# Optimization experiments

Hardware: AMD Instinct MI355X
Metric: run time of the kernel (lower is better)

Reference implementation:

```python
import jax, jax.numpy as jnp
import numpy as np

D_MODEL = 768
N_HEADS = 12
HEAD_DIM = D_MODEL // N_HEADS
NEG = -10000.0


def setup_inputs() -> dict:
    key = jax.random.key(0)
    ks = jax.random.split(key, 8)
    B, S, D = 2, 2048, D_MODEL
    inp = {
        "q": jax.random.normal(ks[0], (B, S, D), dtype=jnp.float32),
        "k": jax.random.normal(ks[1], (B, S, D), dtype=jnp.float32),
        "v": jax.random.normal(ks[2], (B, S, D), dtype=jnp.float32),
        "attn_mask": jax.random.randint(ks[3], (B, S), 0, 2, dtype=jnp.int32),
        # weights stored [in, out]; apply as x @ W (equivalent to torch Linear)
        "Wq": jax.random.normal(ks[4], (D, D), dtype=jnp.float32) / np.sqrt(D),
        "Wk": jax.random.normal(ks[5], (D, D), dtype=jnp.float32) / np.sqrt(D),
        "Wv": jax.random.normal(ks[6], (D, D), dtype=jnp.float32) / np.sqrt(D),
        "Wo": jax.random.normal(ks[7], (D, D), dtype=jnp.float32) / np.sqrt(D),
        "mask_future": 1,
    }
    return inp


def reference(q, k, v, attn_mask, Wq, Wk, Wv, Wo, mask_future):
    B, S, D = q.shape
    H, hd = N_HEADS, HEAD_DIM
    # project and split heads -> [B, H, S, hd]
    qh = (q @ Wq).reshape(B, S, H, hd).transpose(0, 2, 1, 3)
    kh = (k @ Wk).reshape(B, S, H, hd).transpose(0, 2, 1, 3)
    vh = (v @ Wv).reshape(B, S, H, hd).transpose(0, 2, 1, 3)

    scale = 1.0 / np.sqrt(hd).astype(np.float32)
    # full [B, H, L, S] score matrix (naive SDPA, as in the original)
    scores = jnp.einsum("bhld,bhsd->bhls", qh, kh) * scale
    if mask_future:
        causal = jnp.triu(jnp.full((S, S), NEG, dtype=scores.dtype), k=1)
        scores = scores + causal
    # padding mask: [B, S] -> broadcast over heads and query positions
    pad = attn_mask[:, None, None, :] == 0
    scores = jnp.where(pad, NEG, scores)
    attn = jax.nn.softmax(scores, axis=-1)  # dropout p=0.0 -> identity
    out = jnp.einsum("bhls,bhsd->bhld", attn, vh)  # [B, H, L, hd]
    out = out.transpose(0, 2, 1, 3).reshape(B, S, D)
    return out @ Wo
```

## Files before the change

### kernel.cpp

```cpp
#include <hip/hip_runtime.h>


#define NEGV (-10000.0f)

typedef __attribute__((ext_vector_type(8))) short v8s;
typedef __attribute__((ext_vector_type(4))) float v4f;
typedef __attribute__((ext_vector_type(8))) unsigned short v8u;

#define GLDS16(g, l)                                            \
  __builtin_amdgcn_global_load_lds(                             \
      (const __attribute__((address_space(1))) void*)(g),       \
      (__attribute__((address_space(3))) void*)(l), 16, 0, 0)

#define BAR()                                                   \
  do {                                                          \
    asm volatile("s_waitcnt lgkmcnt(0)" ::: "memory");          \
    __builtin_amdgcn_s_barrier();                               \
    __builtin_amdgcn_sched_barrier(0);                          \
  } while (0)

__device__ __forceinline__ unsigned short f2bf(float f) {
  unsigned int u = __float_as_uint(f);
  u += 0x7FFFu + ((u >> 16) & 1u);
  return (unsigned short)(u >> 16);
}

__device__ __forceinline__ unsigned int cvt_pk_bf16(float lo, float hi) {
  unsigned int r;
  asm("v_cvt_pk_bf16_f32 %0, %1, %2" : "=v"(r) : "v"(lo), "v"(hi));
  return r;
}

__global__ __launch_bounds__(256) void transpose_w(
    const float* __restrict__ w0, const float* __restrict__ w1,
    const float* __restrict__ w2, const float* __restrict__ w3,
    unsigned short* __restrict__ t0, unsigned short* __restrict__ t1,
    unsigned short* __restrict__ t2, unsigned short* __restrict__ t3) {
  const float* w; unsigned short* t;
  switch (blockIdx.z) {
    case 0: w = w0; t = t0; break;
    case 1: w = w1; t = t1; break;
    case 2: w = w2; t = t2; break;
    default: w = w3; t = t3; break;
  }
  __shared__ unsigned short tile[32][33];
  const int tx = threadIdx.x & 31, ty = threadIdx.x >> 5;
  const int x0 = blockIdx.x * 32, y0 = blockIdx.y * 32;
#pragma unroll
  for (int j = 0; j < 4; j++)
    tile[ty + j * 8][tx] = f2bf(w[(size_t)(y0 + ty + j * 8) * 768 + x0 + tx]);
  __syncthreads();
#pragma unroll
  for (int j = 0; j < 4; j++)
    t[(size_t)(x0 + ty + j * 8) * 768 + y0 + tx] = tile[tx][ty + j * 8];
}

__global__ __launch_bounds__(256) void transpose_vh(
    const unsigned short* __restrict__ vh, unsigned short* __restrict__ vht) {
  __shared__ unsigned short tile[32][33];
  const size_t hoff = (size_t)blockIdx.z * 2048 * 64;
  const unsigned short* src = vh + hoff;
  unsigned short* dst = vht + hoff;
  const int s0 = blockIdx.x * 32, d0 = blockIdx.y * 32;
  const int tx = threadIdx.x & 31, ty = threadIdx.x >> 5;
#pragma unroll
  for (int j = 0; j < 4; j++)
    tile[ty + j * 8][tx] = src[(size_t)(s0 + ty + j * 8) * 64 + d0 + tx];
  __syncthreads();
#pragma unroll
  for (int j = 0; j < 4; j++)
    dst[(size_t)(d0 + ty + j * 8) * 2048 + s0 + tx] = tile[tx][ty + j * 8];
}

template <bool ABF16HEAD, bool CF32ROW>
__device__ __forceinline__ void gemm_core(const void* __restrict__ A,
                                          const unsigned short* __restrict__ Wt,
                                          void* __restrict__ C) {
  const int tid = threadIdx.x;
  const int wave = tid >> 6, lane = tid & 63;
  const int quad = lane >> 4, l16 = lane & 15;
  const int wm = wave >> 1, wn = wave & 1;
  const int bm = blockIdx.x * 128, bn = blockIdx.y * 128;

  __shared__ __align__(16) unsigned short As[2][128 * 32];
  __shared__ __align__(16) unsigned short Bs[2][128 * 32];

  const int r0s = tid >> 2, c0s = (tid & 3) << 3;

  v4f acc[4][4];
#pragma unroll
  for (int i = 0; i < 4; i++)
#pragma unroll
    for (int j = 0; j < 4; j++) acc[i][j] = (v4f){0.f, 0.f, 0.f, 0.f};

  float4 nA00, nA01, nA10, nA11;

  auto issueB = [&](int kt, int nb) {
    const int c = kt * 32 + c0s;
    GLDS16(&Wt[(size_t)(bn + r0s) * 768 + c],
           &Bs[nb][(size_t)(wave * 64) * 8]);
    GLDS16(&Wt[(size_t)(bn + r0s + 64) * 768 + c],
           &Bs[nb][(size_t)(256 + wave * 64) * 8]);
  };
  auto issueA_glds = [&](int kt, int nb) {
    const int c = kt * 32 + c0s;
    const int rg0 = bm + r0s, rg1 = bm + r0s + 64;
    size_t a0 = ((size_t)((rg0 >> 11) * 12 + (c >> 6)) * 2048 +
                 (rg0 & 2047)) * 64 + (c & 63);
    size_t a1 = ((size_t)((rg1 >> 11) * 12 + (c >> 6)) * 2048 +
                 (rg1 & 2047)) * 64 + (c & 63);
    GLDS16((const unsigned short*)A + a0, &As[nb][(size_t)(wave * 64) * 8]);
    GLDS16((const unsigned short*)A + a1,
           &As[nb][(size_t)(256 + wave * 64) * 8]);
  };
  auto issueA_f32 = [&](int kt) {
    const float* Af = (const float*)A;
    const int c = kt * 32 + c0s;
    size_t a0 = (size_t)(bm + r0s) * 768 + c;
    size_t a1 = (size_t)(bm + r0s + 64) * 768 + c;
    nA00 = *(const float4*)(Af + a0);
    nA01 = *(const float4*)(Af + a0 + 4);
    nA10 = *(const float4*)(Af + a1);
    nA11 = *(const float4*)(Af + a1 + 4);
  };
  auto writeA_f32 = [&](int nb) {
    v8u t0, t1;
    t0[0] = f2bf(nA00.x); t0[1] = f2bf(nA00.y);
    t0[2] = f2bf(nA00.z); t0[3] = f2bf(nA00.w);
    t0[4] = f2bf(nA01.x); t0[5] = f2bf(nA01.y);
    t0[6] = f2bf(nA01.z); t0[7] = f2bf(nA01.w);
    t1[0] = f2bf(nA10.x); t1[1] = f2bf(nA10.y);
    t1[2] = f2bf(nA10.z); t1[3] = f2bf(nA10.w);
    t1[4] = f2bf(nA11.x); t1[5] = f2bf(nA11.y);
    t1[6] = f2bf(nA11.z); t1[7] = f2bf(nA11.w);
    *(uint4*)&As[nb][r0s * 32 + c0s] = *(uint4*)&t0;
    *(uint4*)&As[nb][(r0s + 64) * 32 + c0s] = *(uint4*)&t1;
  };

  if (ABF16HEAD) {
    issueA_glds(0, 0);
  } else {
    issueA_f32(0);
  }
  issueB(0, 0);
  if (!ABF16HEAD) writeA_f32(0);
  __syncthreads();

  for (int kt = 0; kt < 24; kt++) {
    const int cur = kt & 1, nxt = cur ^ 1;

    if (kt < 23) {
      if (ABF16HEAD) issueA_glds(kt + 1, nxt);
      else issueA_f32(kt + 1);
      issueB(kt + 1, nxt);
    }

    v8s aF[4], bF[4];
#pragma unroll
    for (int mt = 0; mt < 4; mt++)
      aF[mt] =
          *(const v8s*)&As[cur][(wm * 64 + mt * 16 + l16) * 32 + quad * 8];
#pragma unroll
    for (int nt = 0; nt < 4; nt++)
      bF[nt] =
          *(const v8s*)&Bs[cur][(wn * 64 + nt * 16 + l16) * 32 + quad * 8];
#pragma unroll
    for (int mt = 0; mt < 4; mt++)
#pragma unroll
      for (int nt = 0; nt < 4; nt++)
        acc[mt][nt] = __builtin_amdgcn_mfma_f32_16x16x32_bf16(
            aF[mt], bF[nt], acc[mt][nt], 0, 0, 0);

    if (kt < 23 && !ABF16HEAD) writeA_f32(nxt);
    __syncthreads();
  }

#pragma unroll
  for (int mt = 0; mt < 4; mt++) {
#pragma unroll
    for (int i = 0; i < 4; i++) {
      int row = bm + wm * 64 + mt * 16 + quad * 4 + i;
#pragma unroll
      for (int nt = 0; nt < 4; nt++) {
        int col = bn + wn * 64 + nt * 16 + l16;
        if (CF32ROW) {
          ((float*)C)[(size_t)row * 768 + col] = acc[mt][nt][i];
        } else {
          size_t off = ((size_t)((row >> 11) * 12 + (col >> 6)) * 2048 +
                        (row & 2047)) * 64 + (col & 63);
          ((unsigned short*)C)[off] = f2bf(acc[mt][nt][i]);
        }
      }
    }
  }
}

__global__ __launch_bounds__(256) void gemm_qkv(
    const float* __restrict__ xq, const float* __restrict__ xk,
    const float* __restrict__ xv, const unsigned short* __restrict__ wqt,
    const unsigned short* __restrict__ wkt, const unsigned short* __restrict__ wvt,
    unsigned short* __restrict__ qh, unsigned short* __restrict__ kh,
    unsigned short* __restrict__ vh) {
  const float* A; const unsigned short* Wt; unsigned short* C;
  switch (blockIdx.z) {
    case 0: A = xq; Wt = wqt; C = qh; break;
    case 1: A = xk; Wt = wkt; C = kh; break;
    default: A = xv; Wt = wvt; C = vh; break;
  }
  gemm_core<false, false>((const void*)A, Wt, (void*)C);
}

__global__ __launch_bounds__(256) void gemm_o(
    const unsigned short* __restrict__ oat, const unsigned short* __restrict__ wot,
    float* __restrict__ out) {
  gemm_core<true, true>((const void*)oat, wot, (void*)out);
}

__global__ __launch_bounds__(256) void attn_kernel(
    const unsigned short* __restrict__ qh, const unsigned short* __restrict__ kh,
    const unsigned short* __restrict__ vht, const int* __restrict__ attn_mask,
    const int* __restrict__ mask_future, unsigned short* __restrict__ o) {
  const int S = 2048, HD = 64, NH = 12;

  const int nlin = blockIdx.x + 32 * blockIdx.y;
  const int qt = (nlin >> 3) & 31;
  const int bh = (nlin & 7) * 3 + (nlin >> 8);
  const int b = bh / NH, h = bh % NH;

  const int tid = threadIdx.x;
  const int wave = tid >> 6, lane = tid & 63;
  const int quad = lane >> 4, l16 = lane & 15;

  __shared__ __align__(16) unsigned short Ks[2][64 * 72];
  __shared__ __align__(16) unsigned short Vt[2][64 * 72];
  __shared__ __align__(16) unsigned short Ps[4][16 * 72];
  __shared__ int s_flag;

  const size_t head_off = (size_t)(b * NH + h) * S * HD;
  const unsigned short* Kb = kh + head_off;
  const unsigned short* Vb = vht + head_off;

  const int mf = mask_future[0];
  if (tid == 0) s_flag = 0;

  const int qrow_l = qt * 64 + wave * 16 + l16;
  v8s aQ[2];
  {
    const unsigned short* qp = qh + head_off + (size_t)qrow_l * HD + quad * 8;
    aQ[0] = *(const v8s*)(qp);
    aQ[1] = *(const v8s*)(qp + 32);
  }
  const int qbase_D = qt * 64 + wave * 16 + quad * 4;

  float m_i = -1e30f;
  v4f accO[4], accL;
  accL = (v4f){0.f, 0.f, 0.f, 0.f};
#pragma unroll
  for (int dt = 0; dt < 4; dt++) accO[dt] = (v4f){0.f, 0.f, 0.f, 0.f};

  v8s ones;
#pragma unroll
  for (int j = 0; j < 8; j++) ones[j] = (short)0x3F80;

  const int kt_causal = mf ? qt : (S / 64 - 1);
  const int r0 = tid >> 3, c0s = (tid & 7) << 3;

  auto nexttile = [&](int t) -> int {
    if (t < kt_causal) return t + 1;
    if (t == kt_causal) return (mf && kt_causal < S / 64 - 1) ? t + 1 : -1;
    return (t < S / 64 - 1) ? t + 1 : -1;
  };

  uint4 pk0, pk1, pv0, pv1;
  int pmv = 0;
  unsigned long long msk0 = 0, msk1 = 0;
  int rtile = -1, stile = -1;

  auto prefetch = [&](int kt) {
    const uint4* srck = (const uint4*)(Kb + (size_t)kt * 64 * HD);
    pk0 = srck[tid];
    pk1 = srck[256 + tid];
    const unsigned short* vp = Vb + (size_t)r0 * S + kt * 64 + c0s;
    pv0 = *(const uint4*)vp;
    pv1 = *(const uint4*)(vp + (size_t)32 * S);
    pmv = attn_mask[b * S + kt * 64 + lane];
    rtile = kt;
  };

  auto stage = [&](int kb) {
    *(uint4*)&Ks[kb][r0 * 72 + c0s] = pk0;
    *(uint4*)&Ks[kb][(r0 + 32) * 72 + c0s] = pk1;
    *(uint4*)&Vt[kb][r0 * 72 + c0s] = pv0;
    *(uint4*)&Vt[kb][(r0 + 32) * 72 + c0s] = pv1;
    unsigned long long mk = __ballot(pmv != 0);
    if (kb) msk1 = mk; else msk0 = mk;
  };

  for (int phase = 0; phase < 2; phase++) {
    int kt_lo, kt_hi;
    if (phase == 0) { kt_lo = 0; kt_hi = kt_causal; }
    else {
      if (m_i < -5000.f) s_flag = 1;
      __syncthreads();
      if (!s_flag) break;
      kt_lo = kt_causal + 1; kt_hi = S / 64 - 1;
      if (kt_lo > kt_hi) break;
    }

    if (stile != kt_lo) {
      if (rtile != kt_lo) prefetch(kt_lo);
      stage(kt_lo & 1);
      stile = kt_lo;
      int nx = nexttile(kt_lo);
      if (nx >= 0) prefetch(nx);
    }

    for (int kt = kt_lo; kt <= kt_hi; kt++) {
      BAR();

      int nkt = nexttile(kt);
      if (nkt >= 0 && stile != nkt) {
        stage(nkt & 1);
        stile = nkt;
        int n2 = nexttile(nkt);
        if (n2 >= 0) prefetch(n2);
      }

      const int kb = kt & 1;
      const unsigned short* KsB = Ks[kb];
      const unsigned short* VtB = Vt[kb];
      const unsigned long long mk = kb ? msk1 : msk0;

      v4f sc[4];
      __builtin_amdgcn_s_setprio(1);
#pragma unroll
      for (int nt = 0; nt < 4; nt++) {
        const unsigned short* kp = &KsB[(nt * 16 + l16) * 72 + quad * 8];
        v8s k0 = *(const v8s*)kp;
        v8s k1 = *(const v8s*)(kp + 32);
        v4f z = (v4f){0.f, 0.f, 0.f, 0.f};
        z = __builtin_amdgcn_mfma_f32_16x16x32_bf16(k0, aQ[0], z, 0, 0, 0);
        z = __builtin_amdgcn_mfma_f32_16x16x32_bf16(k1, aQ[1], z, 0, 0, 0);
        sc[nt] = z;
      }
      __builtin_amdgcn_s_setprio(0);

#pragma unroll
      for (int nt = 0; nt < 4; nt++) {
#pragma unroll
        for (int i = 0; i < 4; i++) {
          int kid = nt * 16 + quad * 4 + i;
          int key = kt * 64 + kid;
          float v = sc[nt][i] * 0.125f;
          v += (mf && (key > qrow_l)) ? NEGV : 0.f;
          v = ((mk >> kid) & 1ull) ? v : NEGV;
          sc[nt][i] = v;
        }
      }

      float mx;
      {
        float a = fmaxf(fmaxf(sc[0][0], sc[0][1]), fmaxf(sc[0][2], sc[0][3]));
        float b2 = fmaxf(fmaxf(sc[1][0], sc[1][1]), fmaxf(sc[1][2], sc[1][3]));
        float c = fmaxf(fmaxf(sc[2][0], sc[2][1]), fmaxf(sc[2][2], sc[2][3]));
        float d = fmaxf(fmaxf(sc[3][0], sc[3][1]), fmaxf(sc[3][2], sc[3][3]));
        mx = fmaxf(fmaxf(a, b2), fmaxf(c, d));
      }
      mx = fmaxf(mx, __shfl_xor(mx, 16));
      mx = fmaxf(mx, __shfl_xor(mx, 32));

      if (!__all(mx - m_i <= 8.0f)) {
        float mnew = fmaxf(m_i, mx);
        float alpha = __expf(m_i - mnew);
        m_i = mnew;
        float a0 = __shfl(alpha, quad * 4 + 0);
        float a1 = __shfl(alpha, quad * 4 + 1);
        float a2 = __shfl(alpha, quad * 4 + 2);
        float a3 = __shfl(alpha, quad * 4 + 3);
#pragma unroll
        for (int dt = 0; dt < 4; dt++) {
          accO[dt][0] *= a0; accO[dt][1] *= a1;
          accO[dt][2] *= a2; accO[dt][3] *= a3;
        }
        accL[0] *= a0; accL[1] *= a1; accL[2] *= a2; accL[3] *= a3;
      }

#pragma unroll
      for (int nt = 0; nt < 4; nt++) {
#pragma unroll
        for (int i = 0; i < 4; i++)
          sc[nt][i] = __expf(sc[nt][i] - m_i);
        uint2 w;
        w.x = cvt_pk_bf16(sc[nt][0], sc[nt][1]);
        w.y = cvt_pk_bf16(sc[nt][2], sc[nt][3]);
        *(uint2*)&Ps[wave][l16 * 72 + nt * 16 + quad * 4] = w;
      }

      __builtin_amdgcn_s_setprio(1);
#pragma unroll
      for (int ks = 0; ks < 2; ks++) {
        v8s aP = *(const v8s*)&Ps[wave][l16 * 72 + ks * 32 + quad * 8];
        accL = __builtin_amdgcn_mfma_f32_16x16x32_bf16(aP, ones, accL, 0, 0, 0);
#pragma unroll
        for (int dt = 0; dt < 4; dt++) {
          v8s bV = *(const v8s*)&VtB[(dt * 16 + l16) * 72 + ks * 32 + quad * 8];
          accO[dt] =
              __builtin_amdgcn_mfma_f32_16x16x32_bf16(aP, bV, accO[dt], 0, 0, 0);
        }
      }
      __builtin_amdgcn_s_setprio(0);
    }
    if (phase == 0) __syncthreads();
  }

#pragma unroll
  for (int i = 0; i < 4; i++) {
    float inv = 1.f / accL[i];
    int qr = qbase_D + i;
    size_t base = head_off + (size_t)qr * HD;
#pragma unroll
    for (int dt = 0; dt < 4; dt++)
      o[base + dt * 16 + l16] = f2bf(accO[dt][i] * inv);
  }
}

extern "C" void kernel_launch(void* const* d_in, const int* in_sizes, int n_in,
                              void* d_out, int out_size, void* d_ws, size_t ws_size,
                              hipStream_t stream) {
  const float* q  = (const float*)d_in[0];
  const float* k  = (const float*)d_in[1];
  const float* v  = (const float*)d_in[2];
  const int* amask = (const int*)d_in[3];
  const float* Wq = (const float*)d_in[4];
  const float* Wk = (const float*)d_in[5];
  const float* Wv = (const float*)d_in[6];
  const float* Wo = (const float*)d_in[7];
  const int* mf  = (const int*)d_in[8];
  float* out = (float*)d_out;

  unsigned short* ws = (unsigned short*)d_ws;
  unsigned short* qh = ws;
  unsigned short* kh = qh + 3145728;
  unsigned short* vh = kh + 3145728;
  unsigned short* wqt = vh + 3145728;
  unsigned short* wkt = wqt + 589824;
  unsigned short* wvt = wkt + 589824;
  unsigned short* wot = wvt + 589824;
  unsigned short* vht = (unsigned short*)d_out;

  transpose_w<<<dim3(24, 24, 4), 256, 0, stream>>>(Wq, Wk, Wv, Wo,
                                                   wqt, wkt, wvt, wot);
  gemm_qkv<<<dim3(32, 6, 3), 256, 0, stream>>>(q, k, v, wqt, wkt, wvt,
                                               qh, kh, vh);
  transpose_vh<<<dim3(64, 2, 24), 256, 0, stream>>>(vh, vht);
  attn_kernel<<<dim3(32, 24), 256, 0, stream>>>(qh, kh, vht, amask, mf, qh);
  gemm_o<<<dim3(32, 6), 256, 0, stream>>>(qh, wot, out);
}
```

Baseline: 215.0 us.

## Schedule attention work items dynamically via atomic counter, longest-first

Replaces the static block-to-tile mapping in the attention kernel with a persistent-style loop that pulls work items from a global atomic counter. Items are ordered so that the longest causal query tiles run first, aiming to balance the triangular workload across CUs. The counter is reset inside the preceding transpose kernel. Each item costs an extra atomic plus a barrier, and blocks that exit early still occupy launch slots.

```diff
diff --git a/kernel.cpp b/kernel.cpp
--- a/kernel.cpp
+++ b/kernel.cpp
@@ -56,7 +56,11 @@
 }
 
 __global__ __launch_bounds__(256) void transpose_vh(
-    const unsigned short* __restrict__ vh, unsigned short* __restrict__ vht) {
+    const unsigned short* __restrict__ vh, unsigned short* __restrict__ vht,
+    int* __restrict__ ctr) {
+  if (blockIdx.x == 0 && blockIdx.y == 0 && blockIdx.z == 0 &&
+      threadIdx.x == 0)
+    *ctr = 0;
   __shared__ unsigned short tile[32][33];
   const size_t hoff = (size_t)blockIdx.z * 2048 * 64;
   const unsigned short* src = vh + hoff;
@@ -219,13 +223,9 @@
 __global__ __launch_bounds__(256) void attn_kernel(
     const unsigned short* __restrict__ qh, const unsigned short* __restrict__ kh,
     const unsigned short* __restrict__ vht, const int* __restrict__ attn_mask,
-    const int* __restrict__ mask_future, unsigned short* __restrict__ o) {
+    const int* __restrict__ mask_future, int* __restrict__ ctr,
+    unsigned short* __restrict__ o) {
   const int S = 2048, HD = 64, NH = 12;
-
-  const int nlin = blockIdx.x + 32 * blockIdx.y;
-  const int qt = (nlin >> 3) & 31;
-  const int bh = (nlin & 7) * 3 + (nlin >> 8);
-  const int b = bh / NH, h = bh % NH;
 
   const int tid = threadIdx.x;
   const int wave = tid >> 6, lane = tid & 63;
@@ -235,192 +235,208 @@
   __shared__ __align__(16) unsigned short Vt[2][64 * 72];
   __shared__ __align__(16) unsigned short Ps[4][16 * 72];
   __shared__ int s_flag;
-
-  const size_t head_off = (size_t)(b * NH + h) * S * HD;
-  const unsigned short* Kb = kh + head_off;
-  const unsigned short* Vb = vht + head_off;
+  __shared__ int s_item;
 
   const int mf = mask_future[0];
-  if (tid == 0) s_flag = 0;
-
-  const int qrow_l = qt * 64 + wave * 16 + l16;
-  v8s aQ[2];
-  {
-    const unsigned short* qp = qh + head_off + (size_t)qrow_l * HD + quad * 8;
-    aQ[0] = *(const v8s*)(qp);
-    aQ[1] = *(const v8s*)(qp + 32);
-  }
-  const int qbase_D = qt * 64 + wave * 16 + quad * 4;
-
-  float m_i = -1e30f;
-  v4f accO[4], accL;
-  accL = (v4f){0.f, 0.f, 0.f, 0.f};
-#pragma unroll
-  for (int dt = 0; dt < 4; dt++) accO[dt] = (v4f){0.f, 0.f, 0.f, 0.f};
+  const int r0 = tid >> 3, c0s = (tid & 7) << 3;
 
   v8s ones;
 #pragma unroll
   for (int j = 0; j < 8; j++) ones[j] = (short)0x3F80;
 
-  const int kt_causal = mf ? qt : (S / 64 - 1);
-  const int r0 = tid >> 3, c0s = (tid & 7) << 3;
-
-  auto nexttile = [&](int t) -> int {
-    if (t < kt_causal) return t + 1;
-    if (t == kt_causal) return (mf && kt_causal < S / 64 - 1) ? t + 1 : -1;
-    return (t < S / 64 - 1) ? t + 1 : -1;
-  };
-
-  uint4 pk0, pk1, pv0, pv1;
-  int pmv = 0;
-  unsigned long long msk0 = 0, msk1 = 0;
-  int rtile = -1, stile = -1;
-
-  auto prefetch = [&](int kt) {
-    const uint4* srck = (const uint4*)(Kb + (size_t)kt * 64 * HD);
-    pk0 = srck[tid];
-    pk1 = srck[256 + tid];
-    const unsigned short* vp = Vb + (size_t)r0 * S + kt * 64 + c0s;
-    pv0 = *(const uint4*)vp;
-    pv1 = *(const uint4*)(vp + (size_t)32 * S);
-    pmv = attn_mask[b * S + kt * 64 + lane];
-    rtile = kt;
-  };
-
-  auto stage = [&](int kb) {
-    *(uint4*)&Ks[kb][r0 * 72 + c0s] = pk0;
-    *(uint4*)&Ks[kb][(r0 + 32) * 72 + c0s] = pk1;
-    *(uint4*)&Vt[kb][r0 * 72 + c0s] = pv0;
-    *(uint4*)&Vt[kb][(r0 + 32) * 72 + c0s] = pv1;
-    unsigned long long mk = __ballot(pmv != 0);
-    if (kb) msk1 = mk; else msk0 = mk;
-  };
-
-  for (int phase = 0; phase < 2; phase++) {
-    int kt_lo, kt_hi;
-    if (phase == 0) { kt_lo = 0; kt_hi = kt_causal; }
-    else {
-      if (m_i < -5000.f) s_flag = 1;
-      __syncthreads();
-      if (!s_flag) break;
-      kt_lo = kt_causal + 1; kt_hi = S / 64 - 1;
-      if (kt_lo > kt_hi) break;
+  while (true) {
+    if (tid == 0) s_item = atomicAdd(ctr, 1);
+    __syncthreads();
+    const int it = s_item;
+    if (it >= 768) break;
+
+    int qt, bh;
+    if (it < 24) { qt = 0; bh = it; }
+    else { int j = it - 24; int r = j / 24; qt = 31 - r; bh = j - r * 24; }
+    const int b = bh / NH, h = bh % NH;
+
+    if (tid == 0) s_flag = 0;
+
+    const size_t head_off = (size_t)(b * NH + h) * S * HD;
+    const unsigned short* Kb = kh + head_off;
+    const unsigned short* Vb = vht + head_off;
+
+    const int qrow_l = qt * 64 + wave * 16 + l16;
+    v8s aQ[2];
+    {
+      const unsigned short* qp = qh + head_off + (size_t)qrow_l * HD + quad * 8;
+      aQ[0] = *(const v8s*)(qp);
+      aQ[1] = *(const v8s*)(qp + 32);
     }
-
-    if (stile != kt_lo) {
-      if (rtile != kt_lo) prefetch(kt_lo);
-      stage(kt_lo & 1);
-      stile = kt_lo;
-      int nx = nexttile(kt_lo);
-      if (nx >= 0) prefetch(nx);
+    const int qbase_D = qt * 64 + wave * 16 + quad * 4;
+
+    float m_i = -1e30f;
+    v4f accO[4], accL;
+    accL = (v4f){0.f, 0.f, 0.f, 0.f};
+#pragma unroll
+    for (int dt = 0; dt < 4; dt++) accO[dt] = (v4f){0.f, 0.f, 0.f, 0.f};
+
+    const int kt_causal = mf ? qt : (S / 64 - 1);
+
+    auto nexttile = [&](int t) -> int {
+      if (t < kt_causal) return t + 1;
+      if (t == kt_causal) return (mf && kt_causal < S / 64 - 1) ? t + 1 : -1;
+      return (t < S / 64 - 1) ? t + 1 : -1;
+    };
+
+    uint4 pk0, pk1, pv0, pv1;
+    int pmv = 0;
+    unsigned long long msk0 = 0, msk1 = 0;
+    int rtile = -1, stile = -1;
+
+    auto prefetch = [&](int kt) {
+      const uint4* srck = (const uint4*)(Kb + (size_t)kt * 64 * HD);
+      pk0 = srck[tid];
+      pk1 = srck[256 + tid];
+      const unsigned short* vp = Vb + (size_t)r0 * S + kt * 64 + c0s;
+      pv0 = *(const uint4*)vp;
+      pv1 = *(const uint4*)(vp + (size_t)32 * S);
+      pmv = attn_mask[b * S + kt * 64 + lane];
+      rtile = kt;
+    };
+
+    auto stage = [&](int kb) {
+      *(uint4*)&Ks[kb][r0 * 72 + c0s] = pk0;
+      *(uint4*)&Ks[kb][(r0 + 32) * 72 + c0s] = pk1;
+      *(uint4*)&Vt[kb][r0 * 72 + c0s] = pv0;
+      *(uint4*)&Vt[kb][(r0 + 32) * 72 + c0s] = pv1;
+      unsigned long long mk = __ballot(pmv != 0);
+      if (kb) msk1 = mk; else msk0 = mk;
+    };
+
+    for (int phase = 0; phase < 2; phase++) {
+      int kt_lo, kt_hi;
+      if (phase == 0) { kt_lo = 0; kt_hi = kt_causal; }
+      else {
+        if (m_i < -5000.f) s_flag = 1;
+        __syncthreads();
+        if (!s_flag) break;
+        kt_lo = kt_causal + 1; kt_hi = S / 64 - 1;
+        if (kt_lo > kt_hi) break;
+      }
+
+      if (stile != kt_lo) {
+        if (rtile != kt_lo) prefetch(kt_lo);
+        stage(kt_lo & 1);
+        stile = kt_lo;
+        int nx = nexttile(kt_lo);
+        if (nx >= 0) prefetch(nx);
+      }
+
+      for (int kt = kt_lo; kt <= kt_hi; kt++) {
+        BAR();
+
+        int nkt = nexttile(kt);
+        if (nkt >= 0 && stile != nkt) {
+          stage(nkt & 1);
+          stile = nkt;
+          int n2 = nexttile(nkt);
+          if (n2 >= 0) prefetch(n2);
+        }
+
+        const int kb = kt & 1;
+        const unsigned short* KsB = Ks[kb];
+        const unsigned short* VtB = Vt[kb];
+        const unsigned long long mk = kb ? msk1 : msk0;
+
+        v4f sc[4];
+        __builtin_amdgcn_s_setprio(1);
+#pragma unroll
+        for (int nt = 0; nt < 4; nt++) {
+          const unsigned short* kp = &KsB[(nt * 16 + l16) * 72 + quad * 8];
+          v8s k0 = *(const v8s*)kp;
+          v8s k1 = *(const v8s*)(kp + 32);
+          v4f z = (v4f){0.f, 0.f, 0.f, 0.f};
+          z = __builtin_amdgcn_mfma_f32_16x16x32_bf16(k0, aQ[0], z, 0, 0, 0);
+          z = __builtin_amdgcn_mfma_f32_16x16x32_bf16(k1, aQ[1], z, 0, 0, 0);
+          sc[nt] = z;
+        }
+        __builtin_amdgcn_s_setprio(0);
+
+#pragma unroll
+        for (int nt = 0; nt < 4; nt++) {
+#pragma unroll
+          for (int i = 0; i < 4; i++) {
+            int kid = nt * 16 + quad * 4 + i;
+            int key = kt * 64 + kid;
+            float v = sc[nt][i] * 0.125f;
+            v += (mf && (key > qrow_l)) ? NEGV : 0.f;
+            v = ((mk >> kid) & 1ull) ? v : NEGV;
+            sc[nt][i] = v;
+          }
+        }
+
+        float mx;
+        {
+          float a = fmaxf(fmaxf(sc[0][0], sc[0][1]), fmaxf(sc[0][2], sc[0][3]));
+          float b2 = fmaxf(fmaxf(sc[1][0], sc[1][1]), fmaxf(sc[1][2], sc[1][3]));
+          float c = fmaxf(fmaxf(sc[2][0], sc[2][1]), fmaxf(sc[2][2], sc[2][3]));
+          float d = fmaxf(fmaxf(sc[3][0], sc[3][1]), fmaxf(sc[3][2], sc[3][3]));
+          mx = fmaxf(fmaxf(a, b2), fmaxf(c, d));
+        }
+        mx = fmaxf(mx, __shfl_xor(mx, 16));
+        mx = fmaxf(mx, __shfl_xor(mx, 32));
+
+        if (!__all(mx - m_i <= 8.0f)) {
+          float mnew = fmaxf(m_i, mx);
+          float alpha = __expf(m_i - mnew);
+          m_i = mnew;
+          float a0 = __shfl(alpha, quad * 4 + 0);
+          float a1 = __shfl(alpha, quad * 4 + 1);
+          float a2 = __shfl(alpha, quad * 4 + 2);
+          float a3 = __shfl(alpha, quad * 4 + 3);
+#pragma unroll
+          for (int dt = 0; dt < 4; dt++) {
+            accO[dt][0] *= a0; accO[dt][1] *= a1;
+            accO[dt][2] *= a2; accO[dt][3] *= a3;
+          }
+          accL[0] *= a0; accL[1] *= a1; accL[2] *= a2; accL[3] *= a3;
+        }
+
+#pragma unroll
+        for (int nt = 0; nt < 4; nt++) {
+#pragma unroll
+          for (int i = 0; i < 4; i++)
+            sc[nt][i] = __expf(sc[nt][i] - m_i);
+          uint2 w;
+          w.x = cvt_pk_bf16(sc[nt][0], sc[nt][1]);
+          w.y = cvt_pk_bf16(sc[nt][2], sc[nt][3]);
+          *(uint2*)&Ps[wave][l16 * 72 + nt * 16 + quad * 4] = w;
+        }
+
+        __builtin_amdgcn_s_setprio(1);
+#pragma unroll
+        for (int ks = 0; ks < 2; ks++) {
+          v8s aP = *(const v8s*)&Ps[wave][l16 * 72 + ks * 32 + quad * 8];
+          accL =
+              __builtin_amdgcn_mfma_f32_16x16x32_bf16(aP, ones, accL, 0, 0, 0);
+#pragma unroll
+          for (int dt = 0; dt < 4; dt++) {
+            v8s bV =
+                *(const v8s*)&VtB[(dt * 16 + l16) * 72 + ks * 32 + quad * 8];
+            accO[dt] = __builtin_amdgcn_mfma_f32_16x16x32_bf16(aP, bV,
+                                                               accO[dt], 0, 0, 0);
+          }
+        }
+        __builtin_amdgcn_s_setprio(0);
+      }
+      if (phase == 0) __syncthreads();
     }
 
-    for (int kt = kt_lo; kt <= kt_hi; kt++) {
-      BAR();
-
-      int nkt = nexttile(kt);
-      if (nkt >= 0 && stile != nkt) {
-        stage(nkt & 1);
-        stile = nkt;
-        int n2 = nexttile(nkt);
-        if (n2 >= 0) prefetch(n2);
-      }
-
-      const int kb = kt & 1;
-      const unsigned short* KsB = Ks[kb];
-      const unsigned short* VtB = Vt[kb];
-      const unsigned long long mk = kb ? msk1 : msk0;
-
-      v4f sc[4];
-      __builtin_amdgcn_s_setprio(1);
-#pragma unroll
-      for (int nt = 0; nt < 4; nt++) {
-        const unsigned short* kp = &KsB[(nt * 16 + l16) * 72 + quad * 8];
-        v8s k0 = *(const v8s*)kp;
-        v8s k1 = *(const v8s*)(kp + 32);
-        v4f z = (v4f){0.f, 0.f, 0.f, 0.f};
-        z = __builtin_amdgcn_mfma_f32_16x16x32_bf16(k0, aQ[0], z, 0, 0, 0);
-        z = __builtin_amdgcn_mfma_f32_16x16x32_bf16(k1, aQ[1], z, 0, 0, 0);
-        sc[nt] = z;
-      }
-      __builtin_amdgcn_s_setprio(0);
-
-#pragma unroll
-      for (int nt = 0; nt < 4; nt++) {
-#pragma unroll
-        for (int i = 0; i < 4; i++) {
-          int kid = nt * 16 + quad * 4 + i;
-          int key = kt * 64 + kid;
-          float v = sc[nt][i] * 0.125f;
-          v += (mf && (key > qrow_l)) ? NEGV : 0.f;
-          v = ((mk >> kid) & 1ull) ? v : NEGV;
-          sc[nt][i] = v;
-        }
-      }
-
-      float mx;
-      {
-        float a = fmaxf(fmaxf(sc[0][0], sc[0][1]), fmaxf(sc[0][2], sc[0][3]));
-        float b2 = fmaxf(fmaxf(sc[1][0], sc[1][1]), fmaxf(sc[1][2], sc[1][3]));
-        float c = fmaxf(fmaxf(sc[2][0], sc[2][1]), fmaxf(sc[2][2], sc[2][3]));
-        float d = fmaxf(fmaxf(sc[3][0], sc[3][1]), fmaxf(sc[3][2], sc[3][3]));
-        mx = fmaxf(fmaxf(a, b2), fmaxf(c, d));
-      }
-      mx = fmaxf(mx, __shfl_xor(mx, 16));
-      mx = fmaxf(mx, __shfl_xor(mx, 32));
-
-      if (!__all(mx - m_i <= 8.0f)) {
-        float mnew = fmaxf(m_i, mx);
-        float alpha = __expf(m_i - mnew);
-        m_i = mnew;
-        float a0 = __shfl(alpha, quad * 4 + 0);
-        float a1 = __shfl(alpha, quad * 4 + 1);
-        float a2 = __shfl(alpha, quad * 4 + 2);
-        float a3 = __shfl(alpha, quad * 4 + 3);
-#pragma unroll
-        for (int dt = 0; dt < 4; dt++) {
-          accO[dt][0] *= a0; accO[dt][1] *= a1;
-          accO[dt][2] *= a2; accO[dt][3] *= a3;
-        }
-        accL[0] *= a0; accL[1] *= a1; accL[2] *= a2; accL[3] *= a3;
-      }
-
-#pragma unroll
-      for (int nt = 0; nt < 4; nt++) {
-#pragma unroll
-        for (int i = 0; i < 4; i++)
-          sc[nt][i] = __expf(sc[nt][i] - m_i);
-        uint2 w;
-        w.x = cvt_pk_bf16(sc[nt][0], sc[nt][1]);
-        w.y = cvt_pk_bf16(sc[nt][2], sc[nt][3]);
-        *(uint2*)&Ps[wave][l16 * 72 + nt * 16 + quad * 4] = w;
-      }
-
-      __builtin_amdgcn_s_setprio(1);
-#pragma unroll
-      for (int ks = 0; ks < 2; ks++) {
-        v8s aP = *(const v8s*)&Ps[wave][l16 * 72 + ks * 32 + quad * 8];
-        accL = __builtin_amdgcn_mfma_f32_16x16x32_bf16(aP, ones, accL, 0, 0, 0);
-#pragma unroll
-        for (int dt = 0; dt < 4; dt++) {
-          v8s bV = *(const v8s*)&VtB[(dt * 16 + l16) * 72 + ks * 32 + quad * 8];
-          accO[dt] =
-              __builtin_amdgcn_mfma_f32_16x16x32_bf16(aP, bV, accO[dt], 0, 0, 0);
-        }
-      }
-      __builtin_amdgcn_s_setprio(0);
+#pragma unroll
+    for (int i = 0; i < 4; i++) {
+      float inv = 1.f / accL[i];
+      int qr = qbase_D + i;
+      size_t base = head_off + (size_t)qr * HD;
+#pragma unroll
+      for (int dt = 0; dt < 4; dt++)
+        o[base + dt * 16 + l16] = f2bf(accO[dt][i] * inv);
     }
-    if (phase == 0) __syncthreads();
-  }
-
-#pragma unroll
-  for (int i = 0; i < 4; i++) {
-    float inv = 1.f / accL[i];
-    int qr = qbase_D + i;
-    size_t base = head_off + (size_t)qr * HD;
-#pragma unroll
-    for (int dt = 0; dt < 4; dt++)
-      o[base + dt * 16 + l16] = f2bf(accO[dt][i] * inv);
   }
 }
 
@@ -446,13 +462,15 @@
   unsigned short* wkt = wqt + 589824;
   unsigned short* wvt = wkt + 589824;
   unsigned short* wot = wvt + 589824;
+  int* ctr = (int*)(wot + 589824);
   unsigned short* vht = (unsigned short*)d_out;
 
   transpose_w<<<dim3(24, 24, 4), 256, 0, stream>>>(Wq, Wk, Wv, Wo,
                                                    wqt, wkt, wvt, wot);
   gemm_qkv<<<dim3(32, 6, 3), 256, 0, stream>>>(q, k, v, wqt, wkt, wvt,
                                                qh, kh, vh);
-  transpose_vh<<<dim3(64, 2, 24), 256, 0, stream>>>(vh, vht);
-  attn_kernel<<<dim3(32, 24), 256, 0, stream>>>(qh, kh, vht, amask, mf, qh);
+  transpose_vh<<<dim3(64, 2, 24), 256, 0, stream>>>(vh, vht, ctr);
+  attn_kernel<<<dim3(32, 24), 256, 0, stream>>>(qh, kh, vht, amask, mf, ctr,
+                                                qh);
   gemm_o<<<dim3(32, 6), 256, 0, stream>>>(qh, wot, out);
 }
```

Measured after the change: 215.2 us. About the same (+0.1%).

## Triple-buffer GEMM tiles with vmcnt-counted barriers and reorder attention block schedule

Applied to the files above, without the earlier changes.

The projection GEMM moves from double to triple buffering of the A and B LDS tiles. It keeps two k-tiles of global loads in flight and waits with partial vmcnt counts instead of full syncs, so load latency hides behind the MFMA work at the cost of more LDS per block. The attention kernel's block-to-(query tile, head) mapping is also changed to issue heavy causal query tiles first, with a serpentine order across waves, to improve load balance.

```diff
diff --git a/kernel.cpp b/kernel.cpp
--- a/kernel.cpp
+++ b/kernel.cpp
@@ -17,6 +17,13 @@
     asm volatile("s_waitcnt lgkmcnt(0)" ::: "memory");          \
     __builtin_amdgcn_s_barrier();                               \
     __builtin_amdgcn_sched_barrier(0);                          \
+  } while (0)
+
+#define GBARN(Nstr)                                                     \
+  do {                                                                  \
+    asm volatile("s_waitcnt vmcnt(" Nstr ") lgkmcnt(0)" ::: "memory");  \
+    __builtin_amdgcn_s_barrier();                                       \
+    __builtin_amdgcn_sched_barrier(0);                                  \
   } while (0)
 
 __device__ __forceinline__ unsigned short f2bf(float f) {
@@ -82,8 +89,8 @@
   const int wm = wave >> 1, wn = wave & 1;
   const int bm = blockIdx.x * 128, bn = blockIdx.y * 128;
 
-  __shared__ __align__(16) unsigned short As[2][128 * 32];
-  __shared__ __align__(16) unsigned short Bs[2][128 * 32];
+  __shared__ __align__(16) unsigned short As[3][128 * 32];
+  __shared__ __align__(16) unsigned short Bs[3][128 * 32];
 
   const int r0s = tid >> 2, c0s = (tid & 3) << 3;
 
@@ -93,7 +100,8 @@
 #pragma unroll
     for (int j = 0; j < 4; j++) acc[i][j] = (v4f){0.f, 0.f, 0.f, 0.f};
 
-  float4 nA00, nA01, nA10, nA11;
+  struct StgA { float4 x0, x1, x2, x3; };
+  StgA sA, sB;
 
   auto issueB = [&](int kt, int nb) {
     const int c = kt * 32 + c0s;
@@ -113,48 +121,30 @@
     GLDS16((const unsigned short*)A + a1,
            &As[nb][(size_t)(256 + wave * 64) * 8]);
   };
-  auto issueA_f32 = [&](int kt) {
+  auto loadF = [&](StgA& s, int kt) {
     const float* Af = (const float*)A;
     const int c = kt * 32 + c0s;
     size_t a0 = (size_t)(bm + r0s) * 768 + c;
     size_t a1 = (size_t)(bm + r0s + 64) * 768 + c;
-    nA00 = *(const float4*)(Af + a0);
-    nA01 = *(const float4*)(Af + a0 + 4);
-    nA10 = *(const float4*)(Af + a1);
-    nA11 = *(const float4*)(Af + a1 + 4);
-  };
-  auto writeA_f32 = [&](int nb) {
+    s.x0 = *(const float4*)(Af + a0);
+    s.x1 = *(const float4*)(Af + a0 + 4);
+    s.x2 = *(const float4*)(Af + a1);
+    s.x3 = *(const float4*)(Af + a1 + 4);
+  };
+  auto writeA = [&](StgA& s, int nb) {
     v8u t0, t1;
-    t0[0] = f2bf(nA00.x); t0[1] = f2bf(nA00.y);
-    t0[2] = f2bf(nA00.z); t0[3] = f2bf(nA00.w);
-    t0[4] = f2bf(nA01.x); t0[5] = f2bf(nA01.y);
-    t0[6] = f2bf(nA01.z); t0[7] = f2bf(nA01.w);
-    t1[0] = f2bf(nA10.x); t1[1] = f2bf(nA10.y);
-    t1[2] = f2bf(nA10.z); t1[3] = f2bf(nA10.w);
-    t1[4] = f2bf(nA11.x); t1[5] = f2bf(nA11.y);
-    t1[6] = f2bf(nA11.z); t1[7] = f2bf(nA11.w);
+    t0[0] = f2bf(s.x0.x); t0[1] = f2bf(s.x0.y);
+    t0[2] = f2bf(s.x0.z); t0[3] = f2bf(s.x0.w);
+    t0[4] = f2bf(s.x1.x); t0[5] = f2bf(s.x1.y);
+    t0[6] = f2bf(s.x1.z); t0[7] = f2bf(s.x1.w);
+    t1[0] = f2bf(s.x2.x); t1[1] = f2bf(s.x2.y);
+    t1[2] = f2bf(s.x2.z); t1[3] = f2bf(s.x2.w);
+    t1[4] = f2bf(s.x3.x); t1[5] = f2bf(s.x3.y);
+    t1[6] = f2bf(s.x3.z); t1[7] = f2bf(s.x3.w);
     *(uint4*)&As[nb][r0s * 32 + c0s] = *(uint4*)&t0;
     *(uint4*)&As[nb][(r0s + 64) * 32 + c0s] = *(uint4*)&t1;
   };
-
-  if (ABF16HEAD) {
-    issueA_glds(0, 0);
-  } else {
-    issueA_f32(0);
-  }
-  issueB(0, 0);
-  if (!ABF16HEAD) writeA_f32(0);
-  __syncthreads();
-
-  for (int kt = 0; kt < 24; kt++) {
-    const int cur = kt & 1, nxt = cur ^ 1;
-
-    if (kt < 23) {
-      if (ABF16HEAD) issueA_glds(kt + 1, nxt);
-      else issueA_f32(kt + 1);
-      issueB(kt + 1, nxt);
-    }
-
+  auto compute = [&](int cur) {
     v8s aF[4], bF[4];
 #pragma unroll
     for (int mt = 0; mt < 4; mt++)
@@ -170,9 +160,46 @@
       for (int nt = 0; nt < 4; nt++)
         acc[mt][nt] = __builtin_amdgcn_mfma_f32_16x16x32_bf16(
             aF[mt], bF[nt], acc[mt][nt], 0, 0, 0);
-
-    if (kt < 23 && !ABF16HEAD) writeA_f32(nxt);
-    __syncthreads();
+  };
+
+  if (ABF16HEAD) {
+    issueA_glds(0, 0); issueB(0, 0);
+    issueA_glds(1, 1); issueB(1, 1);
+    GBARN("4");
+  } else {
+    loadF(sA, 0);
+    loadF(sB, 1);
+    issueB(0, 0); issueB(1, 1);
+    writeA(sA, 0);
+    GBARN("2");
+  }
+
+  for (int kt = 0; kt < 24; kt += 2) {
+    if (kt + 2 < 24) {
+      if (ABF16HEAD) issueA_glds(kt + 2, (kt + 2) % 3);
+      else loadF(sA, kt + 2);
+      issueB(kt + 2, (kt + 2) % 3);
+    }
+    if (!ABF16HEAD) writeA(sB, (kt + 1) % 3);
+    compute(kt % 3);
+    if (kt + 2 < 24) {
+      if (ABF16HEAD) { GBARN("4"); } else { GBARN("6"); }
+    } else {
+      GBARN("0");
+    }
+
+    if (kt + 3 < 24) {
+      if (ABF16HEAD) issueA_glds(kt + 3, (kt + 3) % 3);
+      else loadF(sB, kt + 3);
+      issueB(kt + 3, (kt + 3) % 3);
+    }
+    if (!ABF16HEAD && kt + 2 < 24) writeA(sA, (kt + 2) % 3);
+    compute((kt + 1) % 3);
+    if (kt + 3 < 24) {
+      if (ABF16HEAD) { GBARN("4"); } else { GBARN("6"); }
+    } else {
+      GBARN("0");
+    }
   }
 
 #pragma unroll
@@ -223,8 +250,10 @@
   const int S = 2048, HD = 64, NH = 12;
 
   const int nlin = blockIdx.x + 32 * blockIdx.y;
-  const int qt = (nlin >> 3) & 31;
-  const int bh = (nlin & 7) * 3 + (nlin >> 8);
+  const int m_ = nlin & 255, t_ = nlin >> 8;
+  const int i_ = (t_ == 1) ? (511 - m_) : (t_ * 256 + m_);
+  const int qt = 31 - i_ / 24;
+  const int bh = i_ - (i_ / 24) * 24;
   const int b = bh / NH, h = bh % NH;
 
   const int tid = threadIdx.x;
```

Result: faster. 209.8 us (-2.4%).
